# Performance work log

Measured on AMD Instinct MI355X. Metric: run time of the kernel, lower is better.

The kernel has to match this reference:

```python
import jax, jax.numpy as jnp
import numpy as np

N, C, D = 32, 512, 2048
Q = 64          # num_query_tokens
H = 16          # num_attention_heads
DH = D // H     # head dim


def _mlp(z, w1, b1, w2, b2):
    # projection: Linear(D_r -> D_h), GELU (exact erf, torch default), Linear(D_h -> D_h)
    h = jax.nn.gelu(z @ w1 + b1, approximate=False)
    return h @ w2 + b2


def setup_inputs() -> dict:
    key = jax.random.key(0)
    ks = jax.random.split(key, 16)
    s = 0.02
    inp = {
        "x": jax.random.normal(ks[0], (N, C, D), dtype=jnp.float32),
        # projection MLP (shared by both experts since projector_type has no 'proj')
        "proj_w1": jax.random.normal(ks[1], (D, D), dtype=jnp.float32) * s,
        "proj_b1": jnp.zeros((D,), dtype=jnp.float32),
        "proj_w2": jax.random.normal(ks[2], (D, D), dtype=jnp.float32) * s,
        "proj_b2": jnp.zeros((D,), dtype=jnp.float32),
        # TextResampler (cross-attention with learned queries)
        "query_tokens": jax.random.normal(ks[3], (Q, D), dtype=jnp.float32) * s,
        "wq": jax.random.normal(ks[4], (D, D), dtype=jnp.float32) * s,
        "bq": jnp.zeros((D,), dtype=jnp.float32),
        "wk": jax.random.normal(ks[5], (D, D), dtype=jnp.float32) * s,
        "bk": jnp.zeros((D,), dtype=jnp.float32),
        "wv": jax.random.normal(ks[6], (D, D), dtype=jnp.float32) * s,
        "bv": jnp.zeros((D,), dtype=jnp.float32),
        "wo": jax.random.normal(ks[7], (D, D), dtype=jnp.float32) * s,
        "bo": jnp.zeros((D,), dtype=jnp.float32),
        # gate weight (zeros-init in module; random here to exercise routing)
        "w_gate": jax.random.normal(ks[8], (D, 2), dtype=jnp.float32) * s,
    }
    return inp


def reference(x, proj_w1, proj_b1, proj_w2, proj_b2, query_tokens,
              wq, bq, wk, bk, wv, bv, wo, bo, w_gate):
    n, c, d = x.shape
    # --- sampler: AdaptiveAvgPool2d((Q, D)); D dim is identity, C -> Q block means ---
    x_sampler = x.reshape(n, Q, c // Q, d).mean(axis=2)  # [N, Q, D]

    # --- expert 0: projection MLP on pooled tokens ---
    e0 = _mlp(x_sampler, proj_w1, proj_b1, proj_w2, proj_b2)  # [N, Q, D]

    # --- expert 1: TextResampler cross-attention over x, then shared projection ---
    q = (query_tokens @ wq + bq).reshape(Q, H, DH)            # [Q, H, DH]
    k = (x @ wk + bk).reshape(n, c, H, DH)                    # [N, C, H, DH]
    v = (x @ wv + bv).reshape(n, c, H, DH)
    scores = jnp.einsum("qhd,nchd->nhqc", q, k) / jnp.sqrt(jnp.float32(DH))
    attn = jax.nn.softmax(scores, axis=-1)                    # [N, H, Q, C]
    ctx = jnp.einsum("nhqc,nchd->nqhd", attn, v).reshape(n, Q, d)
    resampled = ctx @ wo + bo                                 # [N, Q, D]
    e1 = _mlp(resampled, proj_w1, proj_b1, proj_w2, proj_b2)  # [N, Q, D]

    # --- noisy top-k gating (eval path: clean logits) ---
    flat = x_sampler.reshape(n * Q, d)
    logits = jax.nn.softmax(flat @ w_gate, axis=1)            # [T, 2]
    top_vals, top_idx = jax.lax.top_k(logits, 2)              # min(k+1, num_experts)=2
    top_k_gates = top_vals / (top_vals.sum(axis=1, keepdims=True) + 1e-6)
    gates = jnp.zeros_like(logits).at[
        jnp.arange(n * Q)[:, None], top_idx].set(top_k_gates)
    gates = gates.reshape(n, Q, 2)

    # --- combine: matmul(stack(experts,-1), gates.unsqueeze(-1)).squeeze(-1) ---
    stacked = jnp.stack([e0, e1], axis=-1)                    # [N, Q, D, E]
    out = jnp.einsum("nqde,nqe->nqd", stacked, gates)
    return out.reshape(-1, d)                                 # [N*Q, D]
```

## Files before the change

kernel.cpp:

```cpp
#include <hip/hip_runtime.h>
#include <hip/hip_bf16.h>

typedef float f32x4 __attribute__((ext_vector_type(4)));
typedef short s16x8 __attribute__((ext_vector_type(8)));
typedef __hip_bfloat16 bf16;

#define NB 32
#define CB 512
#define DB 2048
#define QB 64
#define HB 16
#define DHB 128

static __device__ __forceinline__ void gload16(const void* g, void* l) {
  __builtin_amdgcn_global_load_lds(
      (const __attribute__((address_space(1))) void*)g,
      (__attribute__((address_space(3))) void*)l, 16, 0, 0);
}

static __device__ __forceinline__ unsigned short f2bf(float f) {
  bf16 b = __float2bfloat16(f);
  return *reinterpret_cast<unsigned short*>(&b);
}

static __device__ __forceinline__ float gelu_f(float z) {
  return 0.5f * z * (1.0f + erff(z * 0.7071067811865475f));
}

#define BAR2 do { asm volatile("" ::: "memory"); __builtin_amdgcn_s_barrier(); asm volatile("" ::: "memory"); } while (0)
#define VM2  asm volatile("s_waitcnt vmcnt(2)" ::: "memory")

__global__ void k_convpool(const float* __restrict__ x, bf16* __restrict__ x_bf,
                           bf16* __restrict__ xs) {
  const int d0 = blockIdx.x * 512 + threadIdx.x * 2;
  const int q = blockIdx.y, n = blockIdx.z;
  const size_t base = ((size_t)(n * CB + q * 8)) * DB + d0;
  float s0 = 0.f, s1 = 0.f;
#pragma unroll
  for (int j = 0; j < 8; ++j) {
    float2 v = *(const float2*)(x + base + (size_t)j * DB);
    s0 += v.x; s1 += v.y;
    ushort2 o; o.x = f2bf(v.x); o.y = f2bf(v.y);
    *(ushort2*)((unsigned short*)x_bf + base + (size_t)j * DB) = o;
  }
  ushort2 p; p.x = f2bf(s0 * 0.125f); p.y = f2bf(s1 * 0.125f);
  *(ushort2*)((unsigned short*)xs + ((size_t)(n * QB + q)) * DB + d0) = p;
}

__global__ void k_convert(const float* __restrict__ in, unsigned short* __restrict__ out, int n4) {
  int stride = gridDim.x * blockDim.x;
  for (int i = blockIdx.x * blockDim.x + threadIdx.x; i < n4; i += stride) {
    float4 v = ((const float4*)in)[i];
    ushort4 o;
    o.x = f2bf(v.x); o.y = f2bf(v.y); o.z = f2bf(v.z); o.w = f2bf(v.w);
    ((ushort4*)out)[i] = o;
  }
}

__global__ void k_gate(const bf16* __restrict__ xs, const float* __restrict__ wg,
                       float* __restrict__ gates) {
  int t = blockIdx.x * 4 + (threadIdx.x >> 6);
  int lane = threadIdx.x & 63;
  const bf16* row = xs + (size_t)t * DB;
  float z0 = 0.f, z1 = 0.f;
  for (int d = lane; d < DB; d += 64) {
    float v = __bfloat162float(row[d]);
    z0 += v * wg[d * 2];
    z1 += v * wg[d * 2 + 1];
  }
#pragma unroll
  for (int m = 32; m; m >>= 1) { z0 += __shfl_xor(z0, m, 64); z1 += __shfl_xor(z1, m, 64); }
  if (lane == 0) {
    float mx = fmaxf(z0, z1);
    float e0 = __expf(z0 - mx), e1 = __expf(z1 - mx);
    float s = e0 + e1;
    float p0 = e0 / s, p1 = e1 / s;
    float inv = 1.0f / (p0 + p1 + 1e-6f);
    gates[t * 2] = p0 * inv;
    gates[t * 2 + 1] = p1 * inv;
  }
}

struct TP5 { const float* s[5]; bf16* d[5]; };
__global__ void k_transpose5(TP5 p) {
  __shared__ float t[32][33];
  const float* W = p.s[blockIdx.z];
  bf16* WT = p.d[blockIdx.z];
  int bx = blockIdx.x * 32;
  int by = blockIdx.y * 32;
  int tx = threadIdx.x, ty0 = threadIdx.y;
#pragma unroll
  for (int j = 0; j < 4; ++j) {
    int ty = ty0 + j * 8;
    t[ty][tx] = W[(size_t)(by + ty) * DB + bx + tx];
  }
  __syncthreads();
#pragma unroll
  for (int j = 0; j < 4; ++j) {
    int ty = ty0 + j * 8;
    WT[(size_t)(bx + ty) * DB + by + tx] = __float2bfloat16(t[tx][ty]);
  }
}

template <int EPI>
__global__ __launch_bounds__(512, 2) void k_gemm256(
    const bf16* __restrict__ A, int lda, long long sAb,
    const bf16* __restrict__ BT, int ldb, long long sBb,
    const float* __restrict__ bias, void* __restrict__ Cout, int ldc, long long sCb,
    int K, int ntiles) {
  __shared__ __align__(16) bf16 lds[2][2][256 * 64];

  int bid = blockIdx.x;
  { int c = gridDim.x >> 3; bid = (bid & 7) * c + (bid >> 3); }
  const int m0 = (bid / ntiles) * 256;
  const int n0 = (bid % ntiles) * 256;
  const int z = blockIdx.z;
  A += (size_t)z * sAb;
  BT += (size_t)z * sBb;

  const int tid = threadIdx.x;
  const int l = tid & 63, w = tid >> 6;
  const int wr = w >> 2, wc = w & 3;
  const int fr = l & 15, fg = l >> 4;

  const int rloc = w * 8 + (l >> 3);
  const int cswz = ((l & 7) ^ (l >> 3)) * 8;
  const bf16* Asw = A + cswz;
  const bf16* Bsw = BT + cswz;

  int rbA[4], rbB[4], ckb[2];
#pragma unroll
  for (int mi = 0; mi < 4; ++mi) rbA[mi] = (wr * 64 + mi * 16 + fr) * 128;
#pragma unroll
  for (int ni = 0; ni < 4; ++ni) rbB[ni] = ((ni >> 1) * 128 + wc * 32 + (ni & 1) * 16 + fr) * 128;
#pragma unroll
  for (int kk = 0; kk < 2; ++kk) ckb[kk] = ((kk * 4 + fg) ^ (fr & 7)) * 16;

  f32x4 acc[8][4] = {};
  s16x8 af[4], bfr[4][2];

  auto stg = [&](const bf16* srcsw, int ld, int row0, int kcol, char* dst) {
    gload16(srcsw + (size_t)(row0 + rloc) * ld + kcol, dst + w * 1024);
    gload16(srcsw + (size_t)(row0 + 64 + rloc) * ld + kcol, dst + 8192 + w * 1024);
  };

  stg(Asw, lda, m0, 0, (char*)&lds[0][0][0]);
  stg(Bsw, ldb, n0, 0, (char*)&lds[0][1][0]);
  stg(Bsw, ldb, n0 + 128, 0, (char*)&lds[0][1][0] + 16384);
  stg(Asw, lda, m0 + 128, 0, (char*)&lds[0][0][0] + 16384);
  asm volatile("s_waitcnt vmcnt(0)" ::: "memory");
  BAR2;

  const int NT = K >> 6;
  for (int t = 0; t < NT; ++t) {
    const int buf = t & 1;
    const char* Ab = (const char*)&lds[buf][0][0];
    const char* Bb = (const char*)&lds[buf][1][0];
    char* As = (char*)&lds[buf ^ 1][0][0];
    char* Bs = (char*)&lds[buf ^ 1][1][0];
    const int kn = (t + 1 < NT ? (t + 1) : 0) << 6;

    stg(Asw, lda, m0, kn, As);
#pragma unroll
    for (int mi = 0; mi < 4; ++mi) af[mi] = *(const s16x8*)(Ab + rbA[mi] + ckb[0]);
#pragma unroll
    for (int ni = 0; ni < 4; ++ni) bfr[ni][0] = *(const s16x8*)(Bb + rbB[ni] + ckb[0]);
    __builtin_amdgcn_s_setprio(1);
#pragma unroll
    for (int mi = 0; mi < 4; ++mi)
#pragma unroll
      for (int ni = 0; ni < 4; ++ni)
        acc[mi][ni] = __builtin_amdgcn_mfma_f32_16x16x32_bf16(af[mi], bfr[ni][0], acc[mi][ni], 0, 0, 0);
    __builtin_amdgcn_s_setprio(0);
    VM2;
    BAR2;

    stg(Bsw, ldb, n0, kn, Bs);
#pragma unroll
    for (int mi = 0; mi < 4; ++mi) af[mi] = *(const s16x8*)(Ab + 16384 + rbA[mi] + ckb[0]);
    __builtin_amdgcn_s_setprio(1);
#pragma unroll
    for (int mi = 0; mi < 4; ++mi)
#pragma unroll
      for (int ni = 0; ni < 4; ++ni)
        acc[4 + mi][ni] = __builtin_amdgcn_mfma_f32_16x16x32_bf16(af[mi], bfr[ni][0], acc[4 + mi][ni], 0, 0, 0);
    __builtin_amdgcn_s_setprio(0);

    stg(Bsw, ldb, n0 + 128, kn, Bs + 16384);
#pragma unroll
    for (int mi = 0; mi < 4; ++mi) af[mi] = *(const s16x8*)(Ab + rbA[mi] + ckb[1]);
#pragma unroll
    for (int ni = 0; ni < 4; ++ni) bfr[ni][1] = *(const s16x8*)(Bb + rbB[ni] + ckb[1]);
    __builtin_amdgcn_s_setprio(1);
#pragma unroll
    for (int mi = 0; mi < 4; ++mi)
#pragma unroll
      for (int ni = 0; ni < 4; ++ni)
        acc[mi][ni] = __builtin_amdgcn_mfma_f32_16x16x32_bf16(af[mi], bfr[ni][1], acc[mi][ni], 0, 0, 0);
    __builtin_amdgcn_s_setprio(0);

    stg(Asw, lda, m0 + 128, kn, As + 16384);
#pragma unroll
    for (int mi = 0; mi < 4; ++mi) af[mi] = *(const s16x8*)(Ab + 16384 + rbA[mi] + ckb[1]);
    __builtin_amdgcn_s_setprio(1);
#pragma unroll
    for (int mi = 0; mi < 4; ++mi)
#pragma unroll
      for (int ni = 0; ni < 4; ++ni)
        acc[4 + mi][ni] = __builtin_amdgcn_mfma_f32_16x16x32_bf16(af[mi], bfr[ni][1], acc[4 + mi][ni], 0, 0, 0);
    __builtin_amdgcn_s_setprio(0);
    VM2;
    BAR2;
  }

#pragma unroll
  for (int mi = 0; mi < 8; ++mi) {
    int row = m0 + (mi >> 2) * 128 + wr * 64 + (mi & 3) * 16 + fg * 4;
#pragma unroll
    for (int ni = 0; ni < 4; ++ni) {
      int col = n0 + (ni >> 1) * 128 + wc * 32 + (ni & 1) * 16 + fr;
      float bv = bias ? bias[col] : 0.f;
#pragma unroll
      for (int j = 0; j < 4; ++j) {
        float v = acc[mi][ni][j] + bv;
        size_t o = (size_t)z * sCb + (size_t)(row + j) * ldc + col;
        if (EPI == 0) {
          ((bf16*)Cout)[o] = __float2bfloat16(v);
        } else if (EPI == 1) {
          ((bf16*)Cout)[o] = __float2bfloat16(gelu_f(v));
        } else {
          ((float*)Cout)[o] = v;
        }
      }
    }
  }
}

template <int EPI>
__global__ __launch_bounds__(256) void k_gemm(
    const bf16* __restrict__ A, int lda, long long sAb,
    const bf16* __restrict__ BT, int ldb, long long sBb,
    const float* __restrict__ bias, void* __restrict__ Cout, int ldc, long long sCb,
    int M, int K) {
  __shared__ bf16 As[128 * 32];
  __shared__ bf16 Bs[128 * 32];
  const int z = blockIdx.z;
  A += (size_t)z * sAb;
  BT += (size_t)z * sBb;
  const int tid = threadIdx.x;
  const int lane = tid & 63, w = tid >> 6;
  const int m0 = blockIdx.x * 128, n0 = blockIdx.y * 128;
  const int wm = (w >> 1) * 64, wn = (w & 1) * 64;
  f32x4 acc[4][4] = {};

  const int srow = tid >> 2;
  const int scol = (tid & 3) * 8;
  int gr0 = m0 + srow;       if (gr0 > M - 1) gr0 = M - 1;
  int gr1 = m0 + 64 + srow;  if (gr1 > M - 1) gr1 = M - 1;
  const bf16* ag0 = A + (size_t)gr0 * lda + scol;
  const bf16* ag1 = A + (size_t)gr1 * lda + scol;
  const bf16* bg0 = BT + (size_t)(n0 + srow) * ldb + scol;
  const bf16* bg1 = BT + (size_t)(n0 + 64 + srow) * ldb + scol;
  char* lA = (char*)As + w * 1024;
  char* lB = (char*)Bs + w * 1024;

  const int fr = lane & 15, fk = (lane >> 4) * 8;

  for (int k0 = 0; k0 < K; k0 += 32) {
    __syncthreads();
    gload16(ag0 + k0, lA);
    gload16(ag1 + k0, lA + 4096);
    gload16(bg0 + k0, lB);
    gload16(bg1 + k0, lB + 4096);
    __syncthreads();
    s16x8 af[4], bfr[4];
#pragma unroll
    for (int i = 0; i < 4; ++i)
      af[i] = *(const s16x8*)(As + (wm + i * 16 + fr) * 32 + fk);
#pragma unroll
    for (int i = 0; i < 4; ++i)
      bfr[i] = *(const s16x8*)(Bs + (wn + i * 16 + fr) * 32 + fk);
#pragma unroll
    for (int mi = 0; mi < 4; ++mi)
#pragma unroll
      for (int ni = 0; ni < 4; ++ni)
        acc[mi][ni] = __builtin_amdgcn_mfma_f32_16x16x32_bf16(af[mi], bfr[ni], acc[mi][ni], 0, 0, 0);
  }

  const int fg4 = (lane >> 4) * 4;
#pragma unroll
  for (int mi = 0; mi < 4; ++mi) {
#pragma unroll
    for (int ni = 0; ni < 4; ++ni) {
      int col = n0 + wn + ni * 16 + fr;
      float bv = bias ? bias[col] : 0.f;
#pragma unroll
      for (int j = 0; j < 4; ++j) {
        int r = m0 + wm + mi * 16 + fg4 + j;
        if (r >= M) continue;
        float v = acc[mi][ni][j] + bv;
        size_t o = (size_t)z * sCb + (size_t)r * ldc + col;
        if (EPI == 0) {
          ((bf16*)Cout)[o] = __float2bfloat16(v);
        } else if (EPI == 1) {
          ((bf16*)Cout)[o] = __float2bfloat16(gelu_f(v));
        } else {
          ((float*)Cout)[o] = v;
        }
      }
    }
  }
}

__global__ __launch_bounds__(256) void k_attn(
    const bf16* __restrict__ S, const bf16* __restrict__ Vg, bf16* __restrict__ ctxg) {
  __shared__ bf16 vt[128 * 64];
  __shared__ bf16 pb[4][16 * 64];
  const int nh = blockIdx.x;
  const int n = nh >> 4, h = nh & 15;
  const int tid = threadIdx.x, lane = tid & 63, w = tid >> 6;
  const int fr = lane & 15, fg = lane >> 4;

  f32x4 ctx[8] = {};
  float mrow[4], lrow[4];
#pragma unroll
  for (int j = 0; j < 4; ++j) { mrow[j] = -1e30f; lrow[j] = 0.f; }

  const bf16* Srow = S + ((size_t)n * (HB * QB) + h * QB) * CB;
  const bf16* Vbase = Vg + (size_t)(n * CB) * DB + h * DHB;
  const float SC = 0.08838834764831845f;

  const int krow = tid >> 4;
  const int kcol = (tid & 15) * 8;

  for (int c0 = 0; c0 < CB; c0 += 64) {
    __syncthreads();
#pragma unroll
    for (int jj = 0; jj < 4; ++jj) {
      int row = jj * 16 + krow;
      s16x8 vv = *(const s16x8*)(Vbase + (size_t)(c0 + row) * DB + kcol);
#pragma unroll
      for (int i = 0; i < 8; ++i)
        vt[(kcol + i) * 64 + row] = ((const bf16*)&vv)[i];
    }

    f32x4 s4[4];
#pragma unroll
    for (int ci = 0; ci < 4; ++ci)
#pragma unroll
      for (int j = 0; j < 4; ++j)
        s4[ci][j] = __bfloat162float(Srow[(size_t)(w * 16 + fg * 4 + j) * CB + c0 + ci * 16 + fr]);

#pragma unroll
    for (int j = 0; j < 4; ++j) {
      float m = fmaxf(fmaxf(s4[0][j], s4[1][j]), fmaxf(s4[2][j], s4[3][j])) * SC;
#pragma unroll
      for (int msk = 1; msk < 16; msk <<= 1) m = fmaxf(m, __shfl_xor(m, msk, 16));
      float newm = fmaxf(mrow[j], m);
      float resc = __expf(mrow[j] - newm);
      mrow[j] = newm;
      float rsum = 0.f;
#pragma unroll
      for (int ci = 0; ci < 4; ++ci) {
        float p = __expf(s4[ci][j] * SC - newm);
        rsum += p;
        pb[w][(fg * 4 + j) * 64 + ci * 16 + fr] = __float2bfloat16(p);
      }
#pragma unroll
      for (int msk = 1; msk < 16; msk <<= 1) rsum += __shfl_xor(rsum, msk, 16);
      lrow[j] = lrow[j] * resc + rsum;
#pragma unroll
      for (int ni = 0; ni < 8; ++ni) ctx[ni][j] = ctx[ni][j] * resc;
    }
    __syncthreads();

#pragma unroll
    for (int kk2 = 0; kk2 < 2; ++kk2) {
      s16x8 pa = *(const s16x8*)(&pb[w][fr * 64 + kk2 * 32 + fg * 8]);
#pragma unroll
      for (int ni = 0; ni < 8; ++ni) {
        s16x8 bv = *(const s16x8*)(vt + (ni * 16 + fr) * 64 + kk2 * 32 + fg * 8);
        ctx[ni] = __builtin_amdgcn_mfma_f32_16x16x32_bf16(pa, bv, ctx[ni], 0, 0, 0);
      }
    }
  }

#pragma unroll
  for (int ni = 0; ni < 8; ++ni) {
#pragma unroll
    for (int j = 0; j < 4; ++j) {
      int q = w * 16 + fg * 4 + j;
      float v = ctx[ni][j] / lrow[j];
      ctxg[(size_t)(n * QB + q) * DB + h * DHB + ni * 16 + fr] = __float2bfloat16(v);
    }
  }
}

__global__ void k_combine(const float* __restrict__ e01, const float* __restrict__ gates,
                          float* __restrict__ out) {
  int i = blockIdx.x * blockDim.x + threadIdx.x;
  int t = i >> 9;
  float4 a = ((const float4*)e01)[i];
  float4 b = ((const float4*)e01)[i + (1 << 20)];
  float g0 = gates[t * 2], g1 = gates[t * 2 + 1];
  float4 o;
  o.x = a.x * g0 + b.x * g1;
  o.y = a.y * g0 + b.y * g1;
  o.z = a.z * g0 + b.z * g1;
  o.w = a.w * g0 + b.w * g1;
  ((float4*)out)[i] = o;
}

extern "C" void kernel_launch(void* const* d_in, const int* in_sizes, int n_in,
                              void* d_out, int out_size, void* d_ws, size_t ws_size,
                              hipStream_t stream) {
  const float* x  = (const float*)d_in[0];
  const float* w1 = (const float*)d_in[1];
  const float* b1 = (const float*)d_in[2];
  const float* w2 = (const float*)d_in[3];
  const float* b2 = (const float*)d_in[4];
  const float* qt = (const float*)d_in[5];
  const float* wq = (const float*)d_in[6];
  const float* bq = (const float*)d_in[7];
  const float* wk = (const float*)d_in[8];
  const float* wv = (const float*)d_in[10];
  const float* bv = (const float*)d_in[11];
  const float* wo = (const float*)d_in[12];
  const float* bo = (const float*)d_in[13];
  const float* wg = (const float*)d_in[14];
  float* out = (float*)d_out;

  char* ws = (char*)d_ws;
  size_t off = 0;
  auto alloc = [&](size_t bytes) {
    char* p = ws + off;
    off += (bytes + 255) & ~(size_t)255;
    return p;
  };
  const size_t XE = (size_t)NB * CB * DB;
  const size_t WE = (size_t)DB * DB;
  const size_t TE = (size_t)NB * QB * DB;

  bf16* x_bf   = (bf16*)alloc(XE * 2);
  bf16* V_bf   = (bf16*)alloc(XE * 2);
  bf16* wk_bf  = (bf16*)alloc(WE * 2);
  bf16* w1T    = (bf16*)alloc(WE * 2);
  bf16* w2T    = (bf16*)alloc(WE * 2);
  bf16* wvT    = (bf16*)alloc(WE * 2);
  bf16* wqT    = (bf16*)alloc(WE * 2);
  bf16* woT    = (bf16*)alloc(WE * 2);
  bf16* tokens = (bf16*)alloc(2 * TE * 2);
  bf16* h4     = (bf16*)alloc(2 * TE * 2);
  float* e01   = (float*)alloc(2 * TE * 4);
  bf16* ctx_bf = (bf16*)alloc(TE * 2);
  bf16* qt_bf  = (bf16*)alloc((size_t)QB * DB * 2);
  bf16* qproj  = (bf16*)alloc((size_t)QB * DB * 2);
  bf16* qk     = (bf16*)alloc((size_t)HB * QB * DB * 2);
  bf16* Sbuf   = (bf16*)alloc((size_t)NB * HB * QB * CB * 2);
  float* gates = (float*)alloc((size_t)NB * QB * 2 * 4);
  (void)ws_size; (void)in_sizes; (void)n_in; (void)out_size;

  k_convpool<<<dim3(4, 64, 32), 256, 0, stream>>>(x, x_bf, tokens);
  k_convert<<<64, 256, 0, stream>>>(qt, (unsigned short*)qt_bf, (int)(QB * DB / 4));
  k_convert<<<1024, 256, 0, stream>>>(wk, (unsigned short*)wk_bf, (int)(WE / 4));
  k_gate<<<NB * QB / 4, 256, 0, stream>>>(tokens, wg, gates);

  TP5 tp;
  tp.s[0] = w1; tp.d[0] = w1T;
  tp.s[1] = w2; tp.d[1] = w2T;
  tp.s[2] = wv; tp.d[2] = wvT;
  tp.s[3] = wq; tp.d[3] = wqT;
  tp.s[4] = wo; tp.d[4] = woT;
  k_transpose5<<<dim3(64, 64, 5), dim3(32, 8), 0, stream>>>(tp);

  k_gemm<0><<<dim3(1, 16, 1), 256, 0, stream>>>(
      qt_bf, DB, 0, wqT, DB, 0, bq, qproj, DB, 0, QB, DB);

  k_gemm<0><<<dim3(1, 16, HB), 256, 0, stream>>>(
      qproj, DB, DHB, wk_bf, DB, DHB, nullptr, qk, DB, (long long)QB * DB, QB, DHB);

  k_gemm256<0><<<dim3(512, 1, 1), 512, 0, stream>>>(
      x_bf, DB, 0, wvT, DB, 0, bv, V_bf, DB, 0, DB, 8);

  k_gemm256<0><<<dim3(8, 1, NB), 512, 0, stream>>>(
      qk, DB, 0, x_bf, DB, (long long)CB * DB, nullptr,
      Sbuf, CB, (long long)HB * QB * CB, DB, 2);

  k_attn<<<NB * HB, 256, 0, stream>>>(Sbuf, V_bf, ctx_bf);

  k_gemm256<0><<<dim3(64, 1, 1), 512, 0, stream>>>(
      ctx_bf, DB, 0, woT, DB, 0, bo, tokens + (size_t)2048 * DB, DB, 0, DB, 8);

  k_gemm256<1><<<dim3(128, 1, 1), 512, 0, stream>>>(
      tokens, DB, 0, w1T, DB, 0, b1, h4, DB, 0, DB, 8);
  k_gemm256<2><<<dim3(128, 1, 1), 512, 0, stream>>>(
      h4, DB, 0, w2T, DB, 0, b2, e01, DB, 0, DB, 8);

  k_combine<<<4096, 256, 0, stream>>>(e01, gates, out);
}
```

Baseline: 552.5 us.

## Restructure 256x256 GEMM main loop into four-quadrant ping-pong schedule; switch wo GEMM kernel

Reworks the k_gemm256 inner loop so each phase loads both K sub-slices of the A and B fragments and computes one 128x128 quadrant. Each phase is bracketed by barriers with vmcnt(4) and lgkmcnt(0) waits, so global-to-LDS staging overlaps MFMA work in a ping-pong pattern. The prologue now waits only partially before the first barrier. The wo projection GEMM also moves from the 256-tile kernel (64 blocks) to the smaller-tile k_gemm with 256 blocks to improve occupancy. This adds more barriers and register pressure, and the relaxed prologue wait risks a race if the counts are wrong.

```diff
diff --git a/kernel.cpp b/kernel.cpp
--- a/kernel.cpp
+++ b/kernel.cpp
@@ -27,8 +27,9 @@
   return 0.5f * z * (1.0f + erff(z * 0.7071067811865475f));
 }
 
-#define BAR2 do { asm volatile("" ::: "memory"); __builtin_amdgcn_s_barrier(); asm volatile("" ::: "memory"); } while (0)
-#define VM2  asm volatile("s_waitcnt vmcnt(2)" ::: "memory")
+#define BAR do { asm volatile("" ::: "memory"); __builtin_amdgcn_s_barrier(); asm volatile("" ::: "memory"); } while (0)
+#define VM4 asm volatile("s_waitcnt vmcnt(4)" ::: "memory")
+#define LGK0 do { asm volatile("s_waitcnt lgkmcnt(0)" ::: "memory"); __builtin_amdgcn_sched_barrier(0); } while (0)
 
 __global__ void k_convpool(const float* __restrict__ x, bf16* __restrict__ x_bf,
                            bf16* __restrict__ xs) {
@@ -137,7 +138,7 @@
   for (int kk = 0; kk < 2; ++kk) ckb[kk] = ((kk * 4 + fg) ^ (fr & 7)) * 16;
 
   f32x4 acc[8][4] = {};
-  s16x8 af[4], bfr[4][2];
+  s16x8 af[4][2], afh[4][2], blo[2][2], bhi[2][2];
 
   auto stg = [&](const bf16* srcsw, int ld, int row0, int kcol, char* dst) {
     gload16(srcsw + (size_t)(row0 + rloc) * ld + kcol, dst + w * 1024);
@@ -148,8 +149,8 @@
   stg(Bsw, ldb, n0, 0, (char*)&lds[0][1][0]);
   stg(Bsw, ldb, n0 + 128, 0, (char*)&lds[0][1][0] + 16384);
   stg(Asw, lda, m0 + 128, 0, (char*)&lds[0][0][0] + 16384);
-  asm volatile("s_waitcnt vmcnt(0)" ::: "memory");
-  BAR2;
+  VM4;
+  BAR;
 
   const int NT = K >> 6;
   for (int t = 0; t < NT; ++t) {
@@ -160,57 +161,81 @@
     char* Bs = (char*)&lds[buf ^ 1][1][0];
     const int kn = (t + 1 < NT ? (t + 1) : 0) << 6;
 
+#pragma unroll
+    for (int mi = 0; mi < 4; ++mi)
+#pragma unroll
+      for (int kk = 0; kk < 2; ++kk)
+        af[mi][kk] = *(const s16x8*)(Ab + rbA[mi] + ckb[kk]);
+#pragma unroll
+    for (int ni = 0; ni < 2; ++ni)
+#pragma unroll
+      for (int kk = 0; kk < 2; ++kk)
+        blo[ni][kk] = *(const s16x8*)(Bb + rbB[ni] + ckb[kk]);
     stg(Asw, lda, m0, kn, As);
-#pragma unroll
-    for (int mi = 0; mi < 4; ++mi) af[mi] = *(const s16x8*)(Ab + rbA[mi] + ckb[0]);
-#pragma unroll
-    for (int ni = 0; ni < 4; ++ni) bfr[ni][0] = *(const s16x8*)(Bb + rbB[ni] + ckb[0]);
+    BAR;
+    LGK0;
     __builtin_amdgcn_s_setprio(1);
 #pragma unroll
     for (int mi = 0; mi < 4; ++mi)
 #pragma unroll
-      for (int ni = 0; ni < 4; ++ni)
-        acc[mi][ni] = __builtin_amdgcn_mfma_f32_16x16x32_bf16(af[mi], bfr[ni][0], acc[mi][ni], 0, 0, 0);
+      for (int ni = 0; ni < 2; ++ni)
+#pragma unroll
+        for (int kk = 0; kk < 2; ++kk)
+          acc[mi][ni] = __builtin_amdgcn_mfma_f32_16x16x32_bf16(af[mi][kk], blo[ni][kk], acc[mi][ni], 0, 0, 0);
     __builtin_amdgcn_s_setprio(0);
-    VM2;
-    BAR2;
-
+    VM4;
+    BAR;
+
+#pragma unroll
+    for (int ni = 0; ni < 2; ++ni)
+#pragma unroll
+      for (int kk = 0; kk < 2; ++kk)
+        bhi[ni][kk] = *(const s16x8*)(Bb + rbB[2 + ni] + ckb[kk]);
     stg(Bsw, ldb, n0, kn, Bs);
-#pragma unroll
-    for (int mi = 0; mi < 4; ++mi) af[mi] = *(const s16x8*)(Ab + 16384 + rbA[mi] + ckb[0]);
+    BAR;
+    LGK0;
     __builtin_amdgcn_s_setprio(1);
 #pragma unroll
     for (int mi = 0; mi < 4; ++mi)
 #pragma unroll
-      for (int ni = 0; ni < 4; ++ni)
-        acc[4 + mi][ni] = __builtin_amdgcn_mfma_f32_16x16x32_bf16(af[mi], bfr[ni][0], acc[4 + mi][ni], 0, 0, 0);
+      for (int ni = 0; ni < 2; ++ni)
+#pragma unroll
+        for (int kk = 0; kk < 2; ++kk)
+          acc[mi][2 + ni] = __builtin_amdgcn_mfma_f32_16x16x32_bf16(af[mi][kk], bhi[ni][kk], acc[mi][2 + ni], 0, 0, 0);
     __builtin_amdgcn_s_setprio(0);
-
+    VM4;
+    BAR;
+
+#pragma unroll
+    for (int mi = 0; mi < 4; ++mi)
+#pragma unroll
+      for (int kk = 0; kk < 2; ++kk)
+        afh[mi][kk] = *(const s16x8*)(Ab + 16384 + rbA[mi] + ckb[kk]);
     stg(Bsw, ldb, n0 + 128, kn, Bs + 16384);
-#pragma unroll
-    for (int mi = 0; mi < 4; ++mi) af[mi] = *(const s16x8*)(Ab + rbA[mi] + ckb[1]);
-#pragma unroll
-    for (int ni = 0; ni < 4; ++ni) bfr[ni][1] = *(const s16x8*)(Bb + rbB[ni] + ckb[1]);
+    BAR;
+    LGK0;
     __builtin_amdgcn_s_setprio(1);
 #pragma unroll
     for (int mi = 0; mi < 4; ++mi)
 #pragma unroll
-      for (int ni = 0; ni < 4; ++ni)
-        acc[mi][ni] = __builtin_amdgcn_mfma_f32_16x16x32_bf16(af[mi], bfr[ni][1], acc[mi][ni], 0, 0, 0);
+      for (int ni = 0; ni < 2; ++ni)
+#pragma unroll
+        for (int kk = 0; kk < 2; ++kk)
+          acc[4 + mi][ni] = __builtin_amdgcn_mfma_f32_16x16x32_bf16(afh[mi][kk], blo[ni][kk], acc[4 + mi][ni], 0, 0, 0);
     __builtin_amdgcn_s_setprio(0);
 
     stg(Asw, lda, m0 + 128, kn, As + 16384);
-#pragma unroll
-    for (int mi = 0; mi < 4; ++mi) af[mi] = *(const s16x8*)(Ab + 16384 + rbA[mi] + ckb[1]);
     __builtin_amdgcn_s_setprio(1);
 #pragma unroll
     for (int mi = 0; mi < 4; ++mi)
 #pragma unroll
-      for (int ni = 0; ni < 4; ++ni)
-        acc[4 + mi][ni] = __builtin_amdgcn_mfma_f32_16x16x32_bf16(af[mi], bfr[ni][1], acc[4 + mi][ni], 0, 0, 0);
+      for (int ni = 0; ni < 2; ++ni)
+#pragma unroll
+        for (int kk = 0; kk < 2; ++kk)
+          acc[4 + mi][2 + ni] = __builtin_amdgcn_mfma_f32_16x16x32_bf16(afh[mi][kk], bhi[ni][kk], acc[4 + mi][2 + ni], 0, 0, 0);
     __builtin_amdgcn_s_setprio(0);
-    VM2;
-    BAR2;
+    VM4;
+    BAR;
   }
 
 #pragma unroll
@@ -488,8 +513,8 @@
 
   k_attn<<<NB * HB, 256, 0, stream>>>(Sbuf, V_bf, ctx_bf);
 
-  k_gemm256<0><<<dim3(64, 1, 1), 512, 0, stream>>>(
-      ctx_bf, DB, 0, woT, DB, 0, bo, tokens + (size_t)2048 * DB, DB, 0, DB, 8);
+  k_gemm<0><<<dim3(16, 16, 1), 256, 0, stream>>>(
+      ctx_bf, DB, 0, woT, DB, 0, bo, tokens + (size_t)2048 * DB, DB, 0, 2048, DB);
 
   k_gemm256<1><<<dim3(128, 1, 1), 512, 0, stream>>>(
       tokens, DB, 0, w1T, DB, 0, b1, h4, DB, 0, DB, 8);
```

New measurement: 566.0 us. +2.4%, slower.
